# Kernel tuning notes

Measured on AMD Instinct MI355X. Metric: run time of the kernel, lower is better.

## Reference

```python
import jax, jax.numpy as jnp
import numpy as np

LR_POS = 0.45   # adj_lr_pos: max(i/iters - 1, 0.45) == 0.45 always
LR_SIZE = 0.4
ITERS = 5
BOARD = 640.0


def box_iou(a, b):
    """Pairwise IoU. a: [..., N, 4], b: [..., M, 4] in pascal_voc -> [..., N, M]."""
    area_a = (a[..., 2] - a[..., 0]) * (a[..., 3] - a[..., 1])
    area_b = (b[..., 2] - b[..., 0]) * (b[..., 3] - b[..., 1])
    lt = jnp.maximum(a[..., :, None, :2], b[..., None, :, :2])
    rb = jnp.minimum(a[..., :, None, 2:], b[..., None, :, 2:])
    wh = jnp.clip(rb - lt, 0.0)
    inter = wh[..., 0] * wh[..., 1]
    union = area_a[..., :, None] + area_b[..., None, :] - inter
    return inter / union


def _make_boxes(key, shape, scale):
    # valid pascal_voc boxes: x1<x2, y1<y2
    corners = jax.random.uniform(key, shape[:-1] + (2, 2), dtype=jnp.float32)
    lo = jnp.min(corners, axis=-2)
    hi = jnp.max(corners, axis=-2) + 0.01  # avoid degenerate zero-area boxes
    return jnp.concatenate([lo, hi], axis=-1) * scale


def setup_inputs() -> dict:
    key = jax.random.key(0)
    k1, k2 = jax.random.split(key)
    B, N, M = 64, 1000, 100
    boxes = _make_boxes(k1, (B, N, 4), BOARD)
    gt_boxes = _make_boxes(k2, (B, M, 4), BOARD)
    return {"boxes": boxes, "gt_boxes": gt_boxes}


def reference(boxes, gt_boxes):
    """Batched progressive box adjustment toward best-IoU ground truth.

    boxes: [B, N, 4], gt_boxes: [B, M, 4], both pascal_voc.
    Returns (all_boxes [B, ITERS+1, N, 4], all_sims [B, ITERS+1, N, M]).
    """
    iou0 = box_iou(boxes, gt_boxes)  # [B, N, M]

    def step(carry, _):
        b, iou = carry
        best = jnp.argmax(iou, axis=-1)                                   # [B, N]
        best_gt = jnp.take_along_axis(gt_boxes, best[..., None], axis=1)  # [B, N, 4]
        cur_center = (b[..., :2] + b[..., 2:]) / 2
        gt_center = (best_gt[..., :2] + best_gt[..., 2:]) / 2
        delta_center = gt_center - cur_center
        delta_size = (best_gt[..., 2:] - best_gt[..., :2]) - (b[..., 2:] - b[..., :2])
        new_lt = b[..., :2] + LR_POS * delta_center
        new_rb = b[..., 2:] + LR_POS * delta_center + LR_SIZE * (delta_size - delta_center)
        new_b = jnp.concatenate([new_lt, new_rb], axis=-1)
        new_iou = box_iou(new_b, gt_boxes)
        return (new_b, new_iou), (new_b, new_iou)

    _, (boxes_seq, iou_seq) = jax.lax.scan(step, (boxes, iou0), None, length=ITERS)
    # prepend initial state: [ITERS+1, B, ...] -> [B, ITERS+1, ...]
    all_boxes = jnp.concatenate([boxes[None], boxes_seq], axis=0).transpose(1, 0, 2, 3)
    all_sims = jnp.concatenate([iou0[None], iou_seq], axis=0).transpose(1, 0, 2, 3)
    return all_boxes, all_sims
```

## Files before the change

kernel.cpp:

```cpp
#include <hip/hip_runtime.h>


#define BB 64
#define NN 1000
#define MM 100
#define NITER 5

__global__ __launch_bounds__(256, 8) void dvg_kernel(
    const float* __restrict__ boxes, const float* __restrict__ gt,
    float* __restrict__ out) {
  __shared__ float4 lgt[MM];

  const int tid = threadIdx.x;
  const int wv = tid >> 6;
  const int lane = tid & 63;
  const int g = lane & 7;
  const int r = lane >> 3;
  const int b = blockIdx.x >> 5;
  const int n0 = (blockIdx.x & 31) * 32 + wv * 8;
  const int n = n0 + r;
  const bool vrow = n < NN;
  const int nc = vrow ? n : NN - 1;

  for (int i = tid; i < MM; i += 256)
    lgt[i] = reinterpret_cast<const float4*>(gt)[b * MM + i];
  __syncthreads();

  float areaG[16];
#pragma unroll
  for (int k = 0; k < 4; ++k) {
    if (k < 3 || g == 0) {
#pragma unroll
      for (int c = 0; c < 4; ++c) {
        const float4 q = lgt[32 * k + 4 * g + c];
        float a = (q.z - q.x) * (q.w - q.y);
        asm("" : "+v"(a));
        areaG[4 * k + c] = a;
      }
    }
  }

  const float4 bx = reinterpret_cast<const float4*>(boxes)[b * NN + nc];
  float b0 = bx.x, b1 = bx.y, b2 = bx.z, b3 = bx.w;

  float* __restrict__ outB = out;
  float* __restrict__ outS = out + (size_t)BB * 6 * NN * 4;

  for (int it = 0;; ++it) {
    asm volatile("" ::: "memory");

    float area = (b2 - b0) * (b3 - b1);
    asm("" : "+v"(area));

    float best = -1.0f;
    int bim = 0;
    const size_t obase = (size_t)(b * 6 + it) * NN + n0;
    float* __restrict__ os = outS + (obase + r) * MM;

#pragma unroll
    for (int k = 0; k < 4; ++k) {
      if (k < 3 || g == 0) {
        float4 d;
#pragma unroll
        for (int c = 0; c < 4; ++c) {
          const int m = 32 * k + 4 * g + c;
          const float4 q = lgt[m];
          const float w = fmaxf(fminf(b2, q.z) - fmaxf(b0, q.x), 0.0f);
          const float h = fmaxf(fminf(b3, q.w) - fmaxf(b1, q.y), 0.0f);
          float inter = w * h;
          asm("" : "+v"(inter));
          const float uni = (area + areaG[4 * k + c]) - inter;
          const float val = inter * __builtin_amdgcn_rcpf(uni);
          (&d.x)[c] = val;
          const bool t = val > best;
          best = t ? val : best;
          bim = t ? m : bim;
        }
        if (vrow) *reinterpret_cast<float4*>(os + 32 * k + 4 * g) = d;
      }
    }

    if (vrow && g < 4) {
      const float comp = g == 0 ? b0 : (g == 1 ? b1 : (g == 2 ? b2 : b3));
      outB[obase * 4 + 4 * r + g] = comp;
    }
    if (it == NITER) break;

#pragma unroll
    for (int off = 1; off <= 4; off <<= 1) {
      const float ov = __shfl_xor(best, off, 64);
      const int obi = __shfl_xor(bim, off, 64);
      const bool t = (ov > best) || (ov == best && obi < bim);
      best = t ? ov : best;
      bim = t ? obi : bim;
    }

    const float4 gg = lgt[bim];
    const float dcx = (gg.x + gg.z) * 0.5f - (b0 + b2) * 0.5f;
    const float dcy = (gg.y + gg.w) * 0.5f - (b1 + b3) * 0.5f;
    const float dsx = (gg.z - gg.x) - (b2 - b0);
    const float dsy = (gg.w - gg.y) - (b3 - b1);
    float px = 0.45f * dcx;
    asm("" : "+v"(px));
    float py = 0.45f * dcy;
    asm("" : "+v"(py));
    float qx = 0.4f * (dsx - dcx);
    asm("" : "+v"(qx));
    float qy = 0.4f * (dsy - dcy);
    asm("" : "+v"(qy));
    b0 = b0 + px;
    b1 = b1 + py;
    b2 = (b2 + px) + qx;
    b3 = (b3 + py) + qy;
  }
}

extern "C" void kernel_launch(void* const* d_in, const int* in_sizes, int n_in,
                              void* d_out, int out_size, void* d_ws,
                              size_t ws_size, hipStream_t stream) {
  const float* boxes = (const float*)d_in[0];
  const float* gt = (const float*)d_in[1];
  float* out = (float*)d_out;
  dvg_kernel<<<BB * 32, 256, 0, stream>>>(boxes, gt, out);
}
```

Before: 39.33 us.

## Compute IoU twice to emit fully contiguous coalesced similarity row stores

Splits the IoU output writing from the argmax computation: each wave stashes its 8 boxes in shared memory, then lanes cover the wave's contiguous 800-float output span with linear float4 stores, recomputing IoU from SoA ground-truth arrays in LDS. The original per-row scattered float4 stores (8 lanes per row with 400-byte row stride) are replaced by fully contiguous wave-wide stores to improve write coalescing. The cost is computing the IoU twice (once for storage, once for the argmax) plus extra LDS traffic. The last iteration skips the argmax pass.

Measured after the change: 68.83 us. 1.75x slower.

```diff
diff --git a/kernel.cpp b/kernel.cpp
--- a/kernel.cpp
+++ b/kernel.cpp
@@ -10,34 +10,46 @@
     const float* __restrict__ boxes, const float* __restrict__ gt,
     float* __restrict__ out) {
   __shared__ float4 lgt[MM];
+  __shared__ float gx1[MM], gy1[MM], gx2[MM], gy2[MM];
+  __shared__ float4 bstash[4][8];
 
   const int tid = threadIdx.x;
   const int wv = tid >> 6;
   const int lane = tid & 63;
-  const int g = lane & 7;
+  const int g7 = lane & 7;
   const int r = lane >> 3;
   const int b = blockIdx.x >> 5;
-  const int n0 = (blockIdx.x & 31) * 32 + wv * 8;
-  const int n = n0 + r;
-  const bool vrow = n < NN;
-  const int nc = vrow ? n : NN - 1;
+  const int row0 = (blockIdx.x & 31) * 32;
+  const int n0w = row0 + wv * 8;
+  const bool wvalid = n0w < NN;
+  const int n = n0w + r;
+  const int nc = n < NN ? n : NN - 1;
 
-  for (int i = tid; i < MM; i += 256)
-    lgt[i] = reinterpret_cast<const float4*>(gt)[b * MM + i];
+  for (int i = tid; i < MM; i += 256) {
+    const float4 q = reinterpret_cast<const float4*>(gt)[b * MM + i];
+    lgt[i] = q;
+    gx1[i] = q.x; gy1[i] = q.y; gx2[i] = q.z; gy2[i] = q.w;
+  }
   __syncthreads();
 
   float areaG[16];
 #pragma unroll
-  for (int k = 0; k < 4; ++k) {
-    if (k < 3 || g == 0) {
+  for (int k = 0; k < 4; ++k)
+    if (k < 3 || g7 == 0)
 #pragma unroll
       for (int c = 0; c < 4; ++c) {
-        const float4 q = lgt[32 * k + 4 * g + c];
+        const float4 q = lgt[32 * k + 4 * g7 + c];
         float a = (q.z - q.x) * (q.w - q.y);
         asm("" : "+v"(a));
         areaG[4 * k + c] = a;
       }
-    }
+
+  int rlj[4], mj[4];
+#pragma unroll
+  for (int j = 0; j < 4; ++j) {
+    const int f = j * 256 + lane * 4;
+    rlj[j] = f / 100;
+    mj[j] = f - rlj[j] * 100;
   }
 
   const float4 bx = reinterpret_cast<const float4*>(boxes)[b * NN + nc];
@@ -49,21 +61,60 @@
   for (int it = 0;; ++it) {
     asm volatile("" ::: "memory");
 
+    if (g7 == 0) bstash[wv][r] = make_float4(b0, b1, b2, b3);
+
+    const size_t obase = (size_t)(b * 6 + it) * NN;
+
+    if (wvalid && g7 < 4) {
+      const float comp = g7 == 0 ? b0 : (g7 == 1 ? b1 : (g7 == 2 ? b2 : b3));
+      outB[(obase + n0w + r) * 4 + g7] = comp;
+    }
+
+    if (wvalid) {
+      float* __restrict__ osb = outS + (obase + n0w) * MM;
+#pragma unroll 2
+      for (int j = 0; j < 4; ++j) {
+        if (j < 3 || lane < 8) {
+          const int f = j * 256 + lane * 4;
+          const float4 bq = *reinterpret_cast<const float4*>(&bstash[wv][rlj[j]]);
+          float ba = (bq.z - bq.x) * (bq.w - bq.y);
+          asm("" : "+v"(ba));
+          const int m = mj[j];
+          const float4 X1 = *reinterpret_cast<const float4*>(&gx1[m]);
+          const float4 Y1 = *reinterpret_cast<const float4*>(&gy1[m]);
+          const float4 X2 = *reinterpret_cast<const float4*>(&gx2[m]);
+          const float4 Y2 = *reinterpret_cast<const float4*>(&gy2[m]);
+          float4 d;
+#pragma unroll
+          for (int c = 0; c < 4; ++c) {
+            const float x1 = (&X1.x)[c], y1 = (&Y1.x)[c];
+            const float x2 = (&X2.x)[c], y2 = (&Y2.x)[c];
+            float ag = (x2 - x1) * (y2 - y1);
+            asm("" : "+v"(ag));
+            const float w = fmaxf(fminf(bq.z, x2) - fmaxf(bq.x, x1), 0.0f);
+            const float h = fmaxf(fminf(bq.w, y2) - fmaxf(bq.y, y1), 0.0f);
+            float inter = w * h;
+            asm("" : "+v"(inter));
+            const float uni = (ba + ag) - inter;
+            (&d.x)[c] = inter * __builtin_amdgcn_rcpf(uni);
+          }
+          *reinterpret_cast<float4*>(&osb[f]) = d;
+        }
+      }
+    }
+
+    if (it == NITER) break;
+
     float area = (b2 - b0) * (b3 - b1);
     asm("" : "+v"(area));
-
     float best = -1.0f;
     int bim = 0;
-    const size_t obase = (size_t)(b * 6 + it) * NN + n0;
-    float* __restrict__ os = outS + (obase + r) * MM;
-
 #pragma unroll
     for (int k = 0; k < 4; ++k) {
-      if (k < 3 || g == 0) {
-        float4 d;
+      if (k < 3 || g7 == 0) {
 #pragma unroll
         for (int c = 0; c < 4; ++c) {
-          const int m = 32 * k + 4 * g + c;
+          const int m = 32 * k + 4 * g7 + c;
           const float4 q = lgt[m];
           const float w = fmaxf(fminf(b2, q.z) - fmaxf(b0, q.x), 0.0f);
           const float h = fmaxf(fminf(b3, q.w) - fmaxf(b1, q.y), 0.0f);
@@ -71,21 +122,12 @@
           asm("" : "+v"(inter));
           const float uni = (area + areaG[4 * k + c]) - inter;
           const float val = inter * __builtin_amdgcn_rcpf(uni);
-          (&d.x)[c] = val;
           const bool t = val > best;
           best = t ? val : best;
           bim = t ? m : bim;
         }
-        if (vrow) *reinterpret_cast<float4*>(os + 32 * k + 4 * g) = d;
       }
     }
-
-    if (vrow && g < 4) {
-      const float comp = g == 0 ? b0 : (g == 1 ? b1 : (g == 2 ? b2 : b3));
-      outB[obase * 4 + 4 * r + g] = comp;
-    }
-    if (it == NITER) break;
-
 #pragma unroll
     for (int off = 1; off <= 4; off <<= 1) {
       const float ov = __shfl_xor(best, off, 64);
```
